# Kernel optimization log

Measured on AMD Instinct MI355X. Metric: run time of the kernel, lower is better.

Reference implementation:

```python
import jax, jax.numpy as jnp
import numpy as np

KS = 3          # deformable kernel size
PAD = 1         # zero padding
N = KS * KS     # sample points per pixel


def conv2d(x, w, b=None, padding=1):
    out = jax.lax.conv_general_dilated(
        x, w, (1, 1), [(padding, padding)] * 2,
        dimension_numbers=('NCHW', 'OIHW', 'NCHW'))
    if b is not None:
        out = out + b[None, :, None, None]
    return out


def setup_inputs() -> dict:
    key = jax.random.key(0)
    k0, k1, k2, k3 = jax.random.split(key, 4)
    B, C, H, W, O = 4, 64, 128, 128, 64
    x = jax.random.normal(k0, (B, C, H, W), jnp.float32)
    # p_conv / m_conv are zero-init in the original; use small random weights
    # so offsets/modulation are non-trivial but sampling stays local.
    w_p = jax.random.normal(k1, (2 * N, C, 3, 3), jnp.float32) * 0.01
    b_p = jnp.zeros((2 * N,), jnp.float32)
    w_m = jax.random.normal(k2, (N, C, 3, 3), jnp.float32) * 0.01
    b_m = jnp.zeros((N,), jnp.float32)
    w_conv = jax.random.normal(k3, (O, C, KS, KS), jnp.float32) / np.sqrt(C * N)
    return {'x': x, 'w_p': w_p, 'b_p': b_p, 'w_m': w_m, 'b_m': b_m, 'w_conv': w_conv}


def reference(x, w_p, b_p, w_m, b_m, w_conv):
    B, C, H, W = x.shape
    offset = conv2d(x, w_p, b_p)              # (B, 2N, H, W): first N rows(x), last N cols(y)
    m = jax.nn.sigmoid(conv2d(x, w_m, b_m))   # (B, N, H, W) modulation
    xp = jnp.pad(x, ((0, 0), (0, 0), (PAD, PAD), (PAD, PAD)))  # zero_padding
    Hp, Wp = H + 2 * PAD, W + 2 * PAD

    # p = p_0 + p_n + offset  (coords in padded image, p_0 starts at 1)
    r = (KS - 1) // 2
    pn_x, pn_y = jnp.meshgrid(jnp.arange(-r, r + 1), jnp.arange(-r, r + 1), indexing='ij')
    pn = jnp.concatenate([pn_x.reshape(-1), pn_y.reshape(-1)]).astype(x.dtype)          # (2N,)
    p0_x, p0_y = jnp.meshgrid(jnp.arange(1, H + 1), jnp.arange(1, W + 1), indexing='ij')
    p0 = jnp.concatenate([jnp.tile(p0_x[None], (N, 1, 1)),
                          jnp.tile(p0_y[None], (N, 1, 1))], 0).astype(x.dtype)           # (2N,H,W)
    p = offset + pn[None, :, None, None] + p0[None]
    p = jnp.moveaxis(p, 1, -1)                # (B,H,W,2N)

    fx = jnp.floor(jax.lax.stop_gradient(p[..., :N]))  # p.detach().floor()
    fy = jnp.floor(jax.lax.stop_gradient(p[..., N:]))
    q_lt_x = jnp.clip(fx, 0, Hp - 1).astype(jnp.int32)
    q_lt_y = jnp.clip(fy, 0, Wp - 1).astype(jnp.int32)
    q_rb_x = jnp.clip(fx + 1, 0, Hp - 1).astype(jnp.int32)
    q_rb_y = jnp.clip(fy + 1, 0, Wp - 1).astype(jnp.int32)
    px = jnp.clip(p[..., :N], 0, Hp - 1)
    py = jnp.clip(p[..., N:], 0, Wp - 1)

    # bilinear kernel weights (same algebra as torch version)
    g_lt = (1 + (q_lt_x - px)) * (1 + (q_lt_y - py))
    g_rb = (1 - (q_rb_x - px)) * (1 - (q_rb_y - py))
    g_lb = (1 + (q_lt_x - px)) * (1 - (q_rb_y - py))
    g_rt = (1 - (q_rb_x - px)) * (1 + (q_lt_y - py))

    xf = xp.reshape(B, C, Hp * Wp)

    def gather(qx, qy):
        idx = (qx * Wp + qy).reshape(B, 1, -1)                      # (B,1,H*W*N)
        return jnp.take_along_axis(xf, idx, axis=2).reshape(B, C, H, W, N)

    x_off = (g_lt[:, None] * gather(q_lt_x, q_lt_y)
             + g_rb[:, None] * gather(q_rb_x, q_rb_y)
             + g_lb[:, None] * gather(q_lt_x, q_rb_y)
             + g_rt[:, None] * gather(q_rb_x, q_lt_y))               # (B,C,H,W,N)

    x_off = x_off * jnp.moveaxis(m, 1, -1)[:, None]                  # modulation (DCNv2)

    # _reshape_x_offset + conv(kernel=ks, stride=ks) == einsum over the N samples
    out = jnp.einsum('bchwk,ock->bohw', x_off,
                     w_conv.reshape(w_conv.shape[0], C, N))
    return out
```

## Files before the change

### kernel.cpp

```cpp
#include <hip/hip_runtime.h>
#include <hip/hip_bf16.h>

#define BB 4
#define CC 64
#define HH 128
#define WW 128
#define OO 64
#define NN 9
#define HW 16384
#define HP 130
#define WP 130

#define WPMB_F  0
#define BPM_OFF 9216
#define WCB_F   9248
#define XT_F    27680

typedef __attribute__((ext_vector_type(8))) short s8v;
typedef __attribute__((ext_vector_type(8))) unsigned short u8v;
typedef __attribute__((ext_vector_type(4))) float f4v;

__device__ __forceinline__ unsigned short f2bu(float f) {
    unsigned int b = __float_as_uint(f);
    return (unsigned short)((b + 0x7FFFu + ((b >> 16) & 1u)) >> 16);
}
__device__ __forceinline__ float bu2f(unsigned short u) {
    return __uint_as_float(((unsigned int)u) << 16);
}

__global__ void __launch_bounds__(256) k_pxt(const float* __restrict__ x,
                                             const float* __restrict__ wp,
                                             const float* __restrict__ bp,
                                             const float* __restrict__ wm,
                                             const float* __restrict__ bm,
                                             const float* __restrict__ wcv,
                                             float* __restrict__ ws) {
    int blk = blockIdx.x;
    int t = threadIdx.x;
    if (blk >= 2048) {
        int tid = (blk - 2048) * 256 + t;
        if (tid < 18432) {
            int r = tid / 576;
            int kk = tid % 576;
            int kt = kk >> 6;
            int c = kk & 63;
            int dy = kt / 3, dx = kt % 3;
            float v = 0.f;
            if (r < 18)       v = wp[((r * 64 + c) * 3 + dy) * 3 + dx];
            else if (r < 27)  v = wm[(((r - 18) * 64 + c) * 3 + dy) * 3 + dx];
            ((unsigned short*)(ws + WPMB_F))[tid] = f2bu(v);
        } else if (tid < 18459) {
            int i = tid - 18432;
            ws[BPM_OFF + i] = (i < 18) ? bp[i] : bm[i - 18];
        } else if (tid >= 20480) {
            int d = tid - 20480;
            int o = d / 576;
            int kk = d % 576;
            int kt = kk >> 6;
            int c = kk & 63;
            ((unsigned short*)(ws + WCB_F))[o * 576 + kk] = f2bu(wcv[(o * 64 + c) * 9 + kt]);
        }
        return;
    }
    int b = blk >> 9;
    int hw = (blk & 511) * 32 + (t >> 3);
    int cg = t & 7;
    const float* xb = x + (size_t)b * 64 * HW + hw;
    unsigned short* xt = (unsigned short*)(ws + XT_F);
    float v[8];
#pragma unroll
    for (int j = 0; j < 8; j++) {
        v[j] = xb[(size_t)(cg * 8 + j) * HW];
    }
    u8v o;
#pragma unroll
    for (int j = 0; j < 8; j++) o[j] = f2bu(v[j]);
    *(u8v*)(xt + ((size_t)(b * HW + hw)) * 64 + cg * 8) = o;
}

__global__ void __launch_bounds__(256) k_main(const float* __restrict__ ws,
                                              float* __restrict__ out) {
    __shared__ unsigned short Sld[4][2][16 * 72];
    __shared__ float pxmL[4][3][NN][16];

    int t = threadIdx.x;
    int lane = t & 63;
    int wv = t >> 6;
    int ln15 = lane & 15;
    int quad = lane >> 4;

    int blk = blockIdx.x;
    int b = blk >> 8;
    int hw0 = (blk & 255) * 64 + wv * 16;

    const unsigned short* wpmb = (const unsigned short*)(ws + WPMB_F);
    const unsigned short* wcb = (const unsigned short*)(ws + WCB_F);
    const unsigned short* xtb = (const unsigned short*)(ws + XT_F) + (size_t)b * HW * 64;
    const float* bpm = ws + BPM_OFF;

    int ip = lane >> 2;
    int cg = lane & 3;
    int cbase = cg * 16;
    int ph = (hw0 + ip) >> 7;
    int pw = (hw0 + ip) & 127;

    unsigned short* S0 = &Sld[wv][0][0];
    unsigned short* S1 = &Sld[wv][1][0];
    const u8v z = (u8v){0, 0, 0, 0, 0, 0, 0, 0};

    {
        f4v acc1[2];
        acc1[0] = (f4v){0.f, 0.f, 0.f, 0.f};
        acc1[1] = (f4v){0.f, 0.f, 0.f, 0.f};

        {
            int h2 = ph - 1, w2 = pw - 1;
            bool val = ((unsigned)h2 < 128u) && ((unsigned)w2 < 128u);
            u8v e0 = z, e1 = z;
            if (val) {
                const unsigned short* src = xtb + ((size_t)(h2 * 128 + w2)) * 64 + cbase;
                e0 = *(const u8v*)(src);
                e1 = *(const u8v*)(src + 8);
            }
            *(u8v*)(&S0[ip * 72 + cbase]) = e0;
            *(u8v*)(&S0[ip * 72 + cbase + 8]) = e1;
        }
        __builtin_amdgcn_wave_barrier();

#pragma unroll 1
        for (int kt = 0; kt < 9; kt++) {
            unsigned short* cur = (kt & 1) ? S1 : S0;
            unsigned short* nxt = (kt & 1) ? S0 : S1;
            s8v a00 = *(const s8v*)(wpmb + ln15 * 576 + kt * 64 + quad * 8);
            s8v a01 = *(const s8v*)(wpmb + ln15 * 576 + kt * 64 + 32 + quad * 8);
            s8v a10 = *(const s8v*)(wpmb + (16 + ln15) * 576 + kt * 64 + quad * 8);
            s8v a11 = *(const s8v*)(wpmb + (16 + ln15) * 576 + kt * 64 + 32 + quad * 8);
            u8v n0 = z, n1 = z;
            if (kt < 8) {
                int k2 = kt + 1;
                int dy = k2 / 3, dx = k2 % 3;
                int h2 = ph + dy - 1, w2 = pw + dx - 1;
                bool val = ((unsigned)h2 < 128u) && ((unsigned)w2 < 128u);
                if (val) {
                    const unsigned short* src = xtb + ((size_t)(h2 * 128 + w2)) * 64 + cbase;
                    n0 = *(const u8v*)(src);
                    n1 = *(const u8v*)(src + 8);
                }
            }
            {
                s8v bf0 = *(const s8v*)(&cur[ln15 * 72 + quad * 8]);
                s8v bf1 = *(const s8v*)(&cur[ln15 * 72 + 32 + quad * 8]);
                acc1[0] = __builtin_amdgcn_mfma_f32_16x16x32_bf16(a00, bf0, acc1[0], 0, 0, 0);
                acc1[1] = __builtin_amdgcn_mfma_f32_16x16x32_bf16(a10, bf0, acc1[1], 0, 0, 0);
                acc1[0] = __builtin_amdgcn_mfma_f32_16x16x32_bf16(a01, bf1, acc1[0], 0, 0, 0);
                acc1[1] = __builtin_amdgcn_mfma_f32_16x16x32_bf16(a11, bf1, acc1[1], 0, 0, 0);
            }
            if (kt < 8) {
                *(u8v*)(&nxt[ip * 72 + cbase]) = n0;
                *(u8v*)(&nxt[ip * 72 + cbase + 8]) = n1;
            }
            __builtin_amdgcn_wave_barrier();
        }

        int gp = hw0 + ln15;
        int h = gp >> 7, w = gp & 127;
#pragma unroll
        for (int mt = 0; mt < 2; mt++) {
#pragma unroll
            for (int r = 0; r < 4; r++) {
                int oc = mt * 16 + quad * 4 + r;
                if (oc < 27) {
                    float v = acc1[mt][r] + bpm[oc];
                    if (oc < 9) {
                        int ki = oc / 3;
                        pxmL[wv][0][oc][ln15] = v + (float)(ki - 1) + (float)(h + 1);
                    } else if (oc < 18) {
                        int k = oc - 9;
                        int kj = k % 3;
                        pxmL[wv][1][k][ln15] = v + (float)(kj - 1) + (float)(w + 1);
                    } else {
                        int k = oc - 18;
                        pxmL[wv][2][k][ln15] = 1.f / (1.f + __expf(-v));
                    }
                }
            }
        }
    }
    __builtin_amdgcn_wave_barrier();

    f4v acc[4];
#pragma unroll
    for (int mt = 0; mt < 4; mt++) acc[mt] = (f4v){0.f, 0.f, 0.f, 0.f};

    auto desc = [&](int kt,
                    float& g0, float& g1, float& g2, float& g3,
                    int& o0, int& o1, int& o2, int& o3) {
        float px = pxmL[wv][0][kt][ip];
        float py = pxmL[wv][1][kt][ip];
        float mk = pxmL[wv][2][kt][ip];
        float fx = floorf(px), fy = floorf(py);
        float pxc = fminf(fmaxf(px, 0.f), (float)(HP - 1));
        float pyc = fminf(fmaxf(py, 0.f), (float)(WP - 1));
        int qltx = (int)fminf(fmaxf(fx, 0.f), (float)(HP - 1));
        int qlty = (int)fminf(fmaxf(fy, 0.f), (float)(WP - 1));
        int qrbx = (int)fminf(fmaxf(fx + 1.f, 0.f), (float)(HP - 1));
        int qrby = (int)fminf(fmaxf(fy + 1.f, 0.f), (float)(WP - 1));

        float gltx = 1.f + ((float)qltx - pxc);
        float glty = 1.f + ((float)qlty - pyc);
        float grbx = 1.f - ((float)qrbx - pxc);
        float grby = 1.f - ((float)qrby - pyc);

        bool vlx = (qltx >= 1) && (qltx <= HH);
        bool vly = (qlty >= 1) && (qlty <= WW);
        bool vrx = (qrbx >= 1) && (qrbx <= HH);
        bool vry = (qrby >= 1) && (qrby <= WW);
        g0 = (vlx && vly) ? gltx * glty * mk : 0.f;
        g1 = (vrx && vry) ? grbx * grby * mk : 0.f;
        g2 = (vlx && vry) ? gltx * grby * mk : 0.f;
        g3 = (vrx && vly) ? grbx * glty * mk : 0.f;

        int xlt = min(max(qltx - 1, 0), HH - 1);
        int ylt = min(max(qlty - 1, 0), WW - 1);
        int xrb = min(max(qrbx - 1, 0), HH - 1);
        int yrb = min(max(qrby - 1, 0), WW - 1);
        o0 = (xlt * WW + ylt) * 64 + cbase;
        o1 = (xrb * WW + yrb) * 64 + cbase;
        o2 = (xlt * WW + yrb) * 64 + cbase;
        o3 = (xrb * WW + ylt) * 64 + cbase;
    };

    {
        float g0, g1, g2, g3; int o0, o1, o2, o3;
        desc(0, g0, g1, g2, g3, o0, o1, o2, o3);
        u8v e0a = *(const u8v*)(xtb + o0), e0b = *(const u8v*)(xtb + o0 + 8);
        u8v e1a = *(const u8v*)(xtb + o1), e1b = *(const u8v*)(xtb + o1 + 8);
        u8v e2a = *(const u8v*)(xtb + o2), e2b = *(const u8v*)(xtb + o2 + 8);
        u8v e3a = *(const u8v*)(xtb + o3), e3b = *(const u8v*)(xtb + o3 + 8);
        u8v sva, svb;
#pragma unroll
        for (int j = 0; j < 8; j++) {
            float va = g0 * bu2f(e0a[j]) + g1 * bu2f(e1a[j])
                     + g2 * bu2f(e2a[j]) + g3 * bu2f(e3a[j]);
            float vb = g0 * bu2f(e0b[j]) + g1 * bu2f(e1b[j])
                     + g2 * bu2f(e2b[j]) + g3 * bu2f(e3b[j]);
            sva[j] = f2bu(va);
            svb[j] = f2bu(vb);
        }
        *(u8v*)(&S0[ip * 72 + cbase]) = sva;
        *(u8v*)(&S0[ip * 72 + cbase + 8]) = svb;
    }
    __builtin_amdgcn_wave_barrier();

#pragma unroll 1
    for (int kt = 0; kt < 9; kt++) {
        unsigned short* cur = (kt & 1) ? S1 : S0;
        unsigned short* nxt = (kt & 1) ? S0 : S1;
        s8v A[4][2];
#pragma unroll
        for (int mt = 0; mt < 4; mt++) {
#pragma unroll
            for (int ks = 0; ks < 2; ks++) {
                A[mt][ks] = *(const s8v*)(wcb + (mt * 16 + ln15) * 576 + kt * 64 + ks * 32 + quad * 8);
            }
        }
        float g0 = 0.f, g1 = 0.f, g2 = 0.f, g3 = 0.f;
        u8v e0a, e0b, e1a, e1b, e2a, e2b, e3a, e3b;
        if (kt < 8) {
            int o0, o1, o2, o3;
            desc(kt + 1, g0, g1, g2, g3, o0, o1, o2, o3);
            e0a = *(const u8v*)(xtb + o0); e0b = *(const u8v*)(xtb + o0 + 8);
            e1a = *(const u8v*)(xtb + o1); e1b = *(const u8v*)(xtb + o1 + 8);
            e2a = *(const u8v*)(xtb + o2); e2b = *(const u8v*)(xtb + o2 + 8);
            e3a = *(const u8v*)(xtb + o3); e3b = *(const u8v*)(xtb + o3 + 8);
        }
#pragma unroll
        for (int ks = 0; ks < 2; ks++) {
            s8v bf = *(const s8v*)(&cur[ln15 * 72 + ks * 32 + quad * 8]);
#pragma unroll
            for (int mt = 0; mt < 4; mt++) {
                acc[mt] = __builtin_amdgcn_mfma_f32_16x16x32_bf16(A[mt][ks], bf, acc[mt], 0, 0, 0);
            }
        }
        if (kt < 8) {
            u8v sva, svb;
#pragma unroll
            for (int j = 0; j < 8; j++) {
                float va = g0 * bu2f(e0a[j]) + g1 * bu2f(e1a[j])
                         + g2 * bu2f(e2a[j]) + g3 * bu2f(e3a[j]);
                float vb = g0 * bu2f(e0b[j]) + g1 * bu2f(e1b[j])
                         + g2 * bu2f(e2b[j]) + g3 * bu2f(e3b[j]);
                sva[j] = f2bu(va);
                svb[j] = f2bu(vb);
            }
            *(u8v*)(&nxt[ip * 72 + cbase]) = sva;
            *(u8v*)(&nxt[ip * 72 + cbase + 8]) = svb;
        }
        __builtin_amdgcn_wave_barrier();
    }

    int pix = hw0 + ln15;
    float* ob = out + (size_t)b * (OO * HW) + pix;
#pragma unroll
    for (int mt = 0; mt < 4; mt++) {
#pragma unroll
        for (int r = 0; r < 4; r++) {
            ob[(size_t)(mt * 16 + quad * 4 + r) * HW] = acc[mt][r];
        }
    }
}

extern "C" void kernel_launch(void* const* d_in, const int* in_sizes, int n_in,
                              void* d_out, int out_size, void* d_ws, size_t ws_size,
                              hipStream_t stream) {
    const float* x   = (const float*)d_in[0];
    const float* wp  = (const float*)d_in[1];
    const float* bp  = (const float*)d_in[2];
    const float* wm  = (const float*)d_in[3];
    const float* bm  = (const float*)d_in[4];
    const float* wcv = (const float*)d_in[5];
    float* ws = (float*)d_ws;
    float* out = (float*)d_out;

    hipLaunchKernelGGL(k_pxt, dim3(2272), dim3(256), 0, stream, x, wp, bp, wm, bm, wcv, ws);
    hipLaunchKernelGGL(k_main, dim3(1024), dim3(256), 0, stream, ws, out);
}
```

Baseline: 144.2 us.

## Transpose x to channel-last via shared-memory tile and swizzle block order

The NCHW-to-NHWC bf16 transpose kernel now reads coalesced float4 rows per channel into a shared tile, then writes 16-byte channel vectors. This replaces the old strided per-channel scalar loads. Both kernels also remap block indices so consecutive blocks spread across XCDs, which is meant to improve L2 locality on the multi-die GPU. Each transpose block now handles 64 pixels, so the grid is halved.

```diff
diff --git a/kernel.cpp b/kernel.cpp
--- a/kernel.cpp
+++ b/kernel.cpp
@@ -37,8 +37,8 @@
                                              float* __restrict__ ws) {
     int blk = blockIdx.x;
     int t = threadIdx.x;
-    if (blk >= 2048) {
-        int tid = (blk - 2048) * 256 + t;
+    if (blk >= 1024) {
+        int tid = (blk - 1024) * 256 + t;
         if (tid < 18432) {
             int r = tid / 576;
             int kk = tid % 576;
@@ -62,20 +62,30 @@
         }
         return;
     }
-    int b = blk >> 9;
-    int hw = (blk & 511) * 32 + (t >> 3);
-    int cg = t & 7;
-    const float* xb = x + (size_t)b * 64 * HW + hw;
+    __shared__ unsigned short tile[64][72];
+    int sb = ((blk & 7) << 7) | (blk >> 3);
+    int b = sb >> 8;
+    int hw0 = (sb & 255) * 64;
     unsigned short* xt = (unsigned short*)(ws + XT_F);
-    float v[8];
-#pragma unroll
-    for (int j = 0; j < 8; j++) {
-        v[j] = xb[(size_t)(cg * 8 + j) * HW];
-    }
-    u8v o;
-#pragma unroll
-    for (int j = 0; j < 8; j++) o[j] = f2bu(v[j]);
-    *(u8v*)(xt + ((size_t)(b * HW + hw)) * 64 + cg * 8) = o;
+
+#pragma unroll
+    for (int p = 0; p < 4; p++) {
+        int c = p * 16 + (t >> 4);
+        int h4 = (t & 15) * 4;
+        float4 v = *(const float4*)(x + ((size_t)(b * 64 + c)) * HW + hw0 + h4);
+        tile[h4 + 0][c] = f2bu(v.x);
+        tile[h4 + 1][c] = f2bu(v.y);
+        tile[h4 + 2][c] = f2bu(v.z);
+        tile[h4 + 3][c] = f2bu(v.w);
+    }
+    __syncthreads();
+#pragma unroll
+    for (int p = 0; p < 2; p++) {
+        int hw = p * 32 + (t >> 3);
+        int cb = (t & 7) * 8;
+        u8v o = *(const u8v*)(&tile[hw][cb]);
+        *(u8v*)(xt + ((size_t)(b * HW + hw0 + hw)) * 64 + cb) = o;
+    }
 }
 
 __global__ void __launch_bounds__(256) k_main(const float* __restrict__ ws,
@@ -89,7 +99,8 @@
     int ln15 = lane & 15;
     int quad = lane >> 4;
 
-    int blk = blockIdx.x;
+    int braw = blockIdx.x;
+    int blk = ((braw & 7) << 7) | (braw >> 3);
     int b = blk >> 8;
     int hw0 = (blk & 255) * 64 + wv * 16;
 
@@ -322,6 +333,6 @@
     float* ws = (float*)d_ws;
     float* out = (float*)d_out;
 
-    hipLaunchKernelGGL(k_pxt, dim3(2272), dim3(256), 0, stream, x, wp, bp, wm, bm, wcv, ws);
+    hipLaunchKernelGGL(k_pxt, dim3(1248), dim3(256), 0, stream, x, wp, bp, wm, bm, wcv, ws);
     hipLaunchKernelGGL(k_main, dim3(1024), dim3(256), 0, stream, ws, out);
 }
```

After: 142.5 us. Within noise of the previous version (-1.2%).
